# Kernel tuning notes

Hardware: AMD Instinct MI355X
Metric: run time of the kernel (lower is better)

## Reference

```python
import jax, jax.numpy as jnp
import numpy as np

N_STEPS = 4   # wavelet steps
N_LIFT = 2    # lifting steps per wavelet step
B, N = 512, 65536
TAPS = 3


def setup_inputs() -> dict:
    key = jax.random.key(0)
    k1, k2, k3 = jax.random.split(key, 3)
    x = jax.random.normal(k1, (B, N), dtype=jnp.float32)
    # torch inits these to zeros; use small random values to exercise the math
    P_coeffs = jax.random.normal(k2, (N_STEPS * N_LIFT, TAPS), dtype=jnp.float32) * 0.1
    U_coeffs = jax.random.normal(k3, (N_STEPS * N_LIFT, TAPS), dtype=jnp.float32) * 0.1
    return {"x": x, "P_coeffs": P_coeffs, "U_coeffs": U_coeffs}


def _cconv(x, h):
    # circular convolution: y[n] = sum_k h[k] * x[(n-k) mod N]; h has 3 taps
    return sum(h[k] * jnp.roll(x, k, axis=-1) for k in range(TAPS))


def reference(x, P_coeffs, U_coeffs):
    zs = []
    lowpass = x
    for j in range(N_STEPS):
        # LazyWavelet: even/odd polyphase split
        evens = lowpass[:, 0::2]
        odds = lowpass[:, 1::2]
        # Lifting steps
        for k in range(N_LIFT):
            i = j * N_LIFT + k
            detail = odds - _cconv(evens, P_coeffs[i])
            average = evens + _cconv(detail, U_coeffs[i])
            evens, odds = average, detail
        # Wavelet.forward keeps coeffs[:,0] (average) as z, recurses on coeffs[:,1] (detail)
        zs.append(evens)
        lowpass = odds
    zs.append(lowpass)
    return tuple(zs)
```

## Files before the change

### kernel.cpp

```cpp
#include <hip/hip_runtime.h>

#define BS    256
#define CHUNK 4096
#define HALO  256
#define NN    65536

template<int M>
__device__ __forceinline__ void level_lift(float* lds, int inOff, int npairs,
                                           int avgOff, int detOff,
                                           const float* __restrict__ Pc,
                                           const float* __restrict__ Uc,
                                           int tid) {
  const int W = M + 8;
  float in[2 * (M + 8)];
  const int p0 = M * tid - 8;
#pragma unroll
  for (int i = 0; i < W; ++i) {
    int p = p0 + i;
    p = p < 0 ? 0 : (p >= npairs ? npairs - 1 : p);
    float2 v = *(const float2*)&lds[inOff + 2 * p];
    in[2 * i] = v.x;
    in[2 * i + 1] = v.y;
  }
  const float P0 = Pc[0], P1 = Pc[1], P2 = Pc[2], P3 = Pc[3], P4 = Pc[4], P5 = Pc[5];
  const float U0 = Uc[0], U1 = Uc[1], U2 = Uc[2], U3 = Uc[3], U4 = Uc[4], U5 = Uc[5];
  __syncthreads();
  float e1 = 0, e2 = 0, d1 = 0, d2 = 0, a1 = 0, a2 = 0, f1 = 0, f2 = 0;
#pragma unroll
  for (int i = 0; i < W; ++i) {
    float e0 = in[2 * i], o0 = in[2 * i + 1];
    float d0 = o0 - (P0 * e0 + P1 * e1 + P2 * e2);
    float a0 = e0 + (U0 * d0 + U1 * d1 + U2 * d2);
    float f0 = d0 - (P3 * a0 + P4 * a1 + P5 * a2);
    float b0 = a0 + (U3 * f0 + U4 * f1 + U5 * f2);
    if (i >= 8) {
      int p = p0 + i;
      if (p < npairs) {
        lds[avgOff + p] = b0;
        lds[detOff + p] = f0;
      }
    }
    e2 = e1; e1 = e0; d2 = d1; d1 = d0; a2 = a1; a1 = a0; f2 = f1; f1 = f0;
  }
}

__device__ __forceinline__ void store4(float* dst, const float* src, int n4, int tid) {
  const float4* s = (const float4*)src;
  float4* d = (float4*)dst;
  for (int i = tid; i < n4; i += BS) d[i] = s[i];
}

__global__ __launch_bounds__(BS)
void wavelet_fused_kernel(const float* __restrict__ x,
                          const float* __restrict__ Pc,
                          const float* __restrict__ Uc,
                          float* __restrict__ out) {
  __shared__ __align__(16) float A[CHUNK + HALO];

  const int tid = threadIdx.x;
  const int cx  = blockIdx.x;
  const int row = blockIdx.y;
  const int S   = cx * CHUNK;

  const float4* x4 = (const float4*)(x + (size_t)row * NN);
  const int base4 = ((S - HALO) & (NN - 1)) >> 2;
  float4* A4 = (float4*)A;
#pragma unroll
  for (int i = tid; i < (CHUNK + HALO) / 4; i += BS)
    A4[i] = x4[(base4 + i) & (NN / 4 - 1)];
  __syncthreads();

  level_lift<9>(A, 0, 2176, 0, 2176, Pc, Uc, tid);
  __syncthreads();
  store4(out + (size_t)row * 32768 + (S >> 1), A + 128, 512, tid);

  level_lift<5>(A, 2176, 1088, 0, 1088, Pc + 6, Uc + 6, tid);
  __syncthreads();
  store4(out + 16777216 + (size_t)row * 16384 + (S >> 2), A + 64, 256, tid);

  level_lift<3>(A, 1088, 544, 0, 544, Pc + 12, Uc + 12, tid);
  __syncthreads();
  store4(out + 25165824 + (size_t)row * 8192 + (S >> 3), A + 32, 128, tid);

  level_lift<2>(A, 544, 272, 0, 272, Pc + 18, Uc + 18, tid);
  __syncthreads();
  store4(out + 29360128 + (size_t)row * 4096 + (S >> 4), A + 16, 64, tid);
  store4(out + 31457280 + (size_t)row * 4096 + (S >> 4), A + 288, 64, tid);
}

extern "C" void kernel_launch(void* const* d_in, const int* in_sizes, int n_in,
                              void* d_out, int out_size, void* d_ws, size_t ws_size,
                              hipStream_t stream) {
  const float* x  = (const float*)d_in[0];
  const float* Pc = (const float*)d_in[1];
  const float* Uc = (const float*)d_in[2];
  float* out = (float*)d_out;

  dim3 grid(NN / CHUNK, 512, 1);
  dim3 block(BS, 1, 1);
  wavelet_fused_kernel<<<grid, block, 0, stream>>>(x, Pc, Uc, out);
}
```

Baseline: 52.66 us.

## Write wavelet outputs directly to global and ping-pong detail buffers in LDS

Measured after the change: 98.09 us. 86.3% more time.

```diff
diff --git a/kernel.cpp b/kernel.cpp
--- a/kernel.cpp
+++ b/kernel.cpp
@@ -5,49 +5,51 @@
 #define HALO  256
 #define NN    65536
 
-template<int M>
-__device__ __forceinline__ void level_lift(float* lds, int inOff, int npairs,
-                                           int avgOff, int detOff,
-                                           const float* __restrict__ Pc,
-                                           const float* __restrict__ Uc,
-                                           int tid) {
-  const int W = M + 8;
-  float in[2 * (M + 8)];
+template<int M, int T, bool SYNC, bool DET_LDS>
+__device__ __forceinline__ void level_lift(
+    float* lds, int inOff, int npairs, int detOff,
+    float* __restrict__ avgG, float* __restrict__ detG, int discard,
+    const float* __restrict__ P6, const float* __restrict__ U6, int tid)
+{
+  constexpr int W = M + 8;
+  const bool act = (T == BS) || (tid < T);
   const int p0 = M * tid - 8;
+  float in[2 * W];
+  if (act) {
 #pragma unroll
-  for (int i = 0; i < W; ++i) {
-    int p = p0 + i;
-    p = p < 0 ? 0 : (p >= npairs ? npairs - 1 : p);
-    float2 v = *(const float2*)&lds[inOff + 2 * p];
-    in[2 * i] = v.x;
-    in[2 * i + 1] = v.y;
+    for (int i = 0; i < W; ++i) {
+      int p = p0 + i;
+      p = p < 0 ? 0 : (p >= npairs ? npairs - 1 : p);
+      float2 v = *(const float2*)&lds[inOff + 2 * p];
+      in[2 * i] = v.x;
+      in[2 * i + 1] = v.y;
+    }
   }
-  const float P0 = Pc[0], P1 = Pc[1], P2 = Pc[2], P3 = Pc[3], P4 = Pc[4], P5 = Pc[5];
-  const float U0 = Uc[0], U1 = Uc[1], U2 = Uc[2], U3 = Uc[3], U4 = Uc[4], U5 = Uc[5];
-  __syncthreads();
-  float e1 = 0, e2 = 0, d1 = 0, d2 = 0, a1 = 0, a2 = 0, f1 = 0, f2 = 0;
+  const float P0 = P6[0], P1 = P6[1], P2 = P6[2], P3 = P6[3], P4 = P6[4], P5 = P6[5];
+  const float U0 = U6[0], U1 = U6[1], U2 = U6[2], U3 = U6[3], U4 = U6[4], U5 = U6[5];
+  if (SYNC) __syncthreads();
+  if (act) {
+    float e1 = 0, e2 = 0, d1 = 0, d2 = 0, a1 = 0, a2 = 0, f1 = 0, f2 = 0;
 #pragma unroll
-  for (int i = 0; i < W; ++i) {
-    float e0 = in[2 * i], o0 = in[2 * i + 1];
-    float d0 = o0 - (P0 * e0 + P1 * e1 + P2 * e2);
-    float a0 = e0 + (U0 * d0 + U1 * d1 + U2 * d2);
-    float f0 = d0 - (P3 * a0 + P4 * a1 + P5 * a2);
-    float b0 = a0 + (U3 * f0 + U4 * f1 + U5 * f2);
-    if (i >= 8) {
-      int p = p0 + i;
-      if (p < npairs) {
-        lds[avgOff + p] = b0;
-        lds[detOff + p] = f0;
+    for (int i = 0; i < W; ++i) {
+      float e0 = in[2 * i], o0 = in[2 * i + 1];
+      float d0 = o0 - (P0 * e0 + P1 * e1 + P2 * e2);
+      float a0 = e0 + (U0 * d0 + U1 * d1 + U2 * d2);
+      float f0 = d0 - (P3 * a0 + P4 * a1 + P5 * a2);
+      float b0 = a0 + (U3 * f0 + U4 * f1 + U5 * f2);
+      if (i >= 8) {
+        int p = p0 + i;
+        if (p < npairs) {
+          if constexpr (DET_LDS) lds[detOff + p] = f0;
+          if (p >= discard) {
+            avgG[p - discard] = b0;
+            if constexpr (!DET_LDS) detG[p - discard] = f0;
+          }
+        }
       }
+      e2 = e1; e1 = e0; d2 = d1; d1 = d0; a2 = a1; a1 = a0; f2 = f1; f1 = f0;
     }
-    e2 = e1; e1 = e0; d2 = d1; d1 = d0; a2 = a1; a1 = a0; f2 = f1; f1 = f0;
   }
-}
-
-__device__ __forceinline__ void store4(float* dst, const float* src, int n4, int tid) {
-  const float4* s = (const float4*)src;
-  float4* d = (float4*)dst;
-  for (int i = tid; i < n4; i += BS) d[i] = s[i];
 }
 
 __global__ __launch_bounds__(BS)
@@ -65,27 +67,26 @@
   const float4* x4 = (const float4*)(x + (size_t)row * NN);
   const int base4 = ((S - HALO) & (NN - 1)) >> 2;
   float4* A4 = (float4*)A;
-#pragma unroll
   for (int i = tid; i < (CHUNK + HALO) / 4; i += BS)
     A4[i] = x4[(base4 + i) & (NN / 4 - 1)];
   __syncthreads();
 
-  level_lift<9>(A, 0, 2176, 0, 2176, Pc, Uc, tid);
+  float* z0 = out + (size_t)row * 32768 + (S >> 1);
+  float* z1 = out + 16777216 + (size_t)row * 16384 + (S >> 2);
+  float* z2 = out + 25165824 + (size_t)row * 8192 + (S >> 3);
+  float* z3 = out + 29360128 + (size_t)row * 4096 + (S >> 4);
+  float* z4 = out + 31457280 + (size_t)row * 4096 + (S >> 4);
+
+  level_lift<9, 256, true, true>(A, 0, 2176, 2176, z0, nullptr, 128, Pc, Uc, tid);
   __syncthreads();
-  store4(out + (size_t)row * 32768 + (S >> 1), A + 128, 512, tid);
 
-  level_lift<5>(A, 2176, 1088, 0, 1088, Pc + 6, Uc + 6, tid);
+  level_lift<9, 128, false, true>(A, 2176, 1088, 0, z1, nullptr, 64, Pc + 6, Uc + 6, tid);
   __syncthreads();
-  store4(out + 16777216 + (size_t)row * 16384 + (S >> 2), A + 64, 256, tid);
 
-  level_lift<3>(A, 1088, 544, 0, 544, Pc + 12, Uc + 12, tid);
+  level_lift<9, 64, false, true>(A, 0, 544, 1088, z2, nullptr, 32, Pc + 12, Uc + 12, tid);
   __syncthreads();
-  store4(out + 25165824 + (size_t)row * 8192 + (S >> 3), A + 32, 128, tid);
 
-  level_lift<2>(A, 544, 272, 0, 272, Pc + 18, Uc + 18, tid);
-  __syncthreads();
-  store4(out + 29360128 + (size_t)row * 4096 + (S >> 4), A + 16, 64, tid);
-  store4(out + 31457280 + (size_t)row * 4096 + (S >> 4), A + 288, 64, tid);
+  level_lift<5, 64, false, false>(A, 1088, 272, 0, z3, z4, 16, Pc + 18, Uc + 18, tid);
 }
 
 extern "C" void kernel_launch(void* const* d_in, const int* in_sizes, int n_in,
```
